# Kernel tuning notes

Hardware: AMD Instinct MI355X
Metric: run time of the kernel (lower is better)

## Reference

```python
import jax, jax.numpy as jnp
import numpy as np

B, T, U, E, INNER, VOCAB = 4, 400, 64, 320, 512, 1024

def setup_inputs() -> dict:
    key = jax.random.key(0)
    k1, k2, k3, k4, k5, k6 = jax.random.split(key, 6)
    enc_state = jax.random.normal(k1, (B, T, E), dtype=jnp.float32)
    dec_state = jax.random.normal(k2, (B, U, E), dtype=jnp.float32)
    # Linear(input_size=2E -> inner): torch stores W as (out, in)
    W1 = jax.random.normal(k3, (INNER, 2 * E), dtype=jnp.float32) * (1.0 / np.sqrt(2 * E))
    b1 = jax.random.normal(k4, (INNER,), dtype=jnp.float32) * 0.01
    W2 = jax.random.normal(k5, (VOCAB, INNER), dtype=jnp.float32) * (1.0 / np.sqrt(INNER))
    b2 = jax.random.normal(k6, (VOCAB,), dtype=jnp.float32) * 0.01
    return {"enc_state": enc_state, "dec_state": dec_state, "W1": W1, "b1": b1, "W2": W2, "b2": b2}

def reference(enc_state, dec_state, W1, b1, W2, b2):
    # Equivalent to: repeat enc to (B,T,U,E), dec to (B,T,U,E), concat -> Linear.
    # concat([enc,dec]) @ W1.T == enc @ W1[:, :E].T + dec @ W1[:, E:].T
    E_ = enc_state.shape[-1]
    enc_proj = jnp.einsum('bte,ie->bti', enc_state, W1[:, :E_])   # (B,T,inner)
    dec_proj = jnp.einsum('bue,ie->bui', dec_state, W1[:, E_:])   # (B,U,inner)
    h = jnp.tanh(enc_proj[:, :, None, :] + dec_proj[:, None, :, :] + b1)  # (B,T,U,inner)
    out = jnp.einsum('btui,vi->btuv', h, W2) + b2                  # (B,T,U,vocab)
    return out
```

## Files before the change

kernel.cpp:

```cpp
#include <hip/hip_runtime.h>

#define B_     4
#define T_     400
#define U_     64
#define E_     320
#define INNER_ 512
#define VOCAB_ 1024
#define M_     (B_ * T_ * U_)
#define BT_    (B_ * T_)
#define NROWS_ (BT_ + B_ * U_)

typedef __attribute__((ext_vector_type(8))) short short8;
typedef __attribute__((ext_vector_type(4))) float f32x4;

__device__ __forceinline__ unsigned short f2bf(float f) {
    union { float f; unsigned u; } v;
    v.f = f;
    unsigned u = v.u;
    u += 0x7fffu + ((u >> 16) & 1u);
    return (unsigned short)(u >> 16);
}

__device__ __forceinline__ float tanh_fast(float x) {
    float e = __expf(2.0f * x);
    return 1.0f - 2.0f / (e + 1.0f);
}

__device__ __forceinline__ void gload_lds16(const void* g, void* l) {
    __builtin_amdgcn_global_load_lds(
        (const __attribute__((address_space(1))) unsigned int*)g,
        (__attribute__((address_space(3))) unsigned int*)l,
        16, 0, 0);
}

#define PROJ_BLOCKS 232
#define CVT_BLOCKS  256

__global__ __launch_bounds__(256) void prep_kernel(
    const float* __restrict__ enc,
    const float* __restrict__ dec,
    const float* __restrict__ W1,
    const float* __restrict__ b1,
    const float* __restrict__ W2,
    float* __restrict__ proj,
    unsigned short* __restrict__ W2bf) {
    __shared__ float xs[8][E_];
    const int tid = threadIdx.x;

    if (blockIdx.x >= PROJ_BLOCKS) {
        const int i = ((blockIdx.x - PROJ_BLOCKS) * 256 + tid) * 8;
        float4 a = *(const float4*)(W2 + i);
        float4 b = *(const float4*)(W2 + i + 4);
        short8 o;
        o[0] = (short)f2bf(a.x); o[1] = (short)f2bf(a.y);
        o[2] = (short)f2bf(a.z); o[3] = (short)f2bf(a.w);
        o[4] = (short)f2bf(b.x); o[5] = (short)f2bf(b.y);
        o[6] = (short)f2bf(b.z); o[7] = (short)f2bf(b.w);
        *(short8*)(W2bf + i) = o;
        return;
    }

    const int r0 = blockIdx.x * 8;
    for (int i = tid; i < 8 * E_; i += 256) {
        const int rr = i / E_;
        const int cc = i - rr * E_;
        const int row = r0 + rr;
        const float* src = (row < BT_) ? (enc + row * E_)
                                       : (dec + (row - BT_) * E_);
        xs[rr][cc] = src[cc];
    }
    const int colbase = (r0 < BT_) ? 0 : E_;
    __syncthreads();

    for (int o = tid; o < INNER_; o += 256) {
        const float* w = W1 + o * (2 * E_) + colbase;
        float acc[8] = {};
        for (int c = 0; c < E_; c += 4) {
            float4 wv = *(const float4*)(w + c);
            #pragma unroll
            for (int rr = 0; rr < 8; ++rr) {
                float4 x = *(const float4*)(&xs[rr][c]);
                acc[rr] += wv.x * x.x + wv.y * x.y + wv.z * x.z + wv.w * x.w;
            }
        }
        const float badd = colbase ? b1[o] : 0.0f;
        #pragma unroll
        for (int rr = 0; rr < 8; ++rr)
            proj[(r0 + rr) * INNER_ + o] = acc[rr] + badd;
    }
}

__global__ __launch_bounds__(256) void hgen_kernel(
    const float* __restrict__ encp,
    const float* __restrict__ decp,
    unsigned short* __restrict__ hbf) {
    const int gid = blockIdx.x * 256 + threadIdx.x;
    const int r   = gid >> 6;
    const int kk  = (gid & 63) << 3;
    const int bt  = r >> 6;
    const int u   = r & 63;
    const int b   = bt / T_;
    const float* e = encp + bt * INNER_ + kk;
    const float* d = decp + (b * U_ + u) * INNER_ + kk;
    short8 o;
    #pragma unroll
    for (int i = 0; i < 2; ++i) {
        float4 e4 = *(const float4*)(e + i * 4);
        float4 d4 = *(const float4*)(d + i * 4);
        o[i * 4 + 0] = (short)f2bf(tanh_fast(e4.x + d4.x));
        o[i * 4 + 1] = (short)f2bf(tanh_fast(e4.y + d4.y));
        o[i * 4 + 2] = (short)f2bf(tanh_fast(e4.z + d4.z));
        o[i * 4 + 3] = (short)f2bf(tanh_fast(e4.w + d4.w));
    }
    *(short8*)(hbf + ((size_t)r << 9) + kk) = o;
}

#define JBM 128
#define JBN 128
#define JBK 32

__global__ __launch_bounds__(256) void joint_gemm_kernel(
    const unsigned short* __restrict__ hbf,
    const unsigned short* __restrict__ W2bf,
    const float* __restrict__ b2,
    float* __restrict__ out) {
    __shared__ unsigned short As[JBM * JBK];
    __shared__ unsigned short Bs[JBN * JBK];

    const int bid = blockIdx.x;
    const int c  = bid & 7;
    const int j  = bid >> 3;
    const int mt = (j & ~7) | c;
    const int nt = j & 7;
    const int m0 = mt * JBM;
    const int n0 = nt * JBN;

    const int tid  = threadIdx.x;
    const int wid  = tid >> 6;
    const int lane = tid & 63;
    const int wm   = (wid & 1) * 64;
    const int wn   = (wid >> 1) * 64;

    const int fr   = lane & 15;
    const int koff = (lane >> 4) * 8;

    f32x4 acc[4][4] = {};

    const char* hbase = (const char*)hbf;
    const char* wbase = (const char*)W2bf;

    for (int kt = 0; kt < INNER_; kt += JBK) {
        const int kb = kt * 2;
        #pragma unroll
        for (int c2 = 0; c2 < 2; ++c2) {
            const int p    = c2 * 4096 + tid * 16;
            const int r    = p >> 6;
            const int off  = p & 63;
            const int ldsb = c2 * 4096 + (wid << 10);
            gload_lds16(hbase + (((size_t)(m0 + r)) << 10) + kb + off,
                        (char*)As + ldsb);
            gload_lds16(wbase + (((size_t)(n0 + r)) << 10) + kb + off,
                        (char*)Bs + ldsb);
        }
        __syncthreads();

        short8 af[4], bfr[4];
        #pragma unroll
        for (int i = 0; i < 4; ++i)
            af[i] = *(const short8*)(As + (wm + fr + i * 16) * JBK + koff);
        #pragma unroll
        for (int i = 0; i < 4; ++i)
            bfr[i] = *(const short8*)(Bs + (wn + fr + i * 16) * JBK + koff);
        #pragma unroll
        for (int im = 0; im < 4; ++im)
            #pragma unroll
            for (int in = 0; in < 4; ++in)
                acc[im][in] = __builtin_amdgcn_mfma_f32_16x16x32_bf16(
                    af[im], bfr[in], acc[im][in], 0, 0, 0);

        __syncthreads();
    }

    const int rq = (lane >> 4) * 4;
    const int cl = lane & 15;
    #pragma unroll
    for (int in = 0; in < 4; ++in) {
        const int col = n0 + wn + in * 16 + cl;
        const float bias = b2[col];
        #pragma unroll
        for (int im = 0; im < 4; ++im) {
            const size_t rbase = (size_t)(m0 + wm + im * 16 + rq);
            #pragma unroll
            for (int r = 0; r < 4; ++r) {
                out[(rbase + r) * VOCAB_ + col] = acc[im][in][r] + bias;
            }
        }
    }
}

#define BM  128
#define BN  128
#define BK  32
#define LDA 40

__global__ __launch_bounds__(256) void joint_fb_kernel(
    const float* __restrict__ encp,
    const float* __restrict__ decp,
    const unsigned short* __restrict__ W2bf,
    const float* __restrict__ b2,
    float* __restrict__ out) {
    __shared__ unsigned short As[BM * LDA];
    __shared__ unsigned short Bs[BN * LDA];

    const int bid = blockIdx.x;
    const int c  = bid & 7;
    const int j  = bid >> 3;
    const int mt = (j & ~7) | c;
    const int nt = j & 7;
    const int m0 = mt * BM;
    const int n0 = nt * BN;

    const int tid  = threadIdx.x;
    const int wid  = tid >> 6;
    const int lane = tid & 63;
    const int wm   = (wid & 1) * 64;
    const int wn   = (wid >> 1) * 64;

    const int sr = tid >> 1;
    const int sk = (tid & 1) * 16;
    const int gr = m0 + sr;
    const int bt = gr >> 6;
    const int uu = gr & 63;
    const int bb = bt / T_;
    const float* eprow = encp + bt * INNER_;
    const float* dprow = decp + (bb * U_ + uu) * INNER_;
    const unsigned short* wrow = W2bf + (size_t)(n0 + sr) * INNER_;

    f32x4 acc[4][4] = {};

    for (int kt = 0; kt < INNER_; kt += BK) {
        const float* ep = eprow + kt + sk;
        const float* dp = dprow + kt + sk;
        short8 p0, p1;
        #pragma unroll
        for (int i = 0; i < 4; ++i) {
            float4 e4 = *(const float4*)(ep + i * 4);
            float4 d4 = *(const float4*)(dp + i * 4);
            unsigned short h0 = f2bf(tanh_fast(e4.x + d4.x));
            unsigned short h1 = f2bf(tanh_fast(e4.y + d4.y));
            unsigned short h2 = f2bf(tanh_fast(e4.z + d4.z));
            unsigned short h3 = f2bf(tanh_fast(e4.w + d4.w));
            if (i < 2) {
                p0[i * 4 + 0] = (short)h0; p0[i * 4 + 1] = (short)h1;
                p0[i * 4 + 2] = (short)h2; p0[i * 4 + 3] = (short)h3;
            } else {
                p1[(i - 2) * 4 + 0] = (short)h0; p1[(i - 2) * 4 + 1] = (short)h1;
                p1[(i - 2) * 4 + 2] = (short)h2; p1[(i - 2) * 4 + 3] = (short)h3;
            }
        }
        *(short8*)(As + sr * LDA + sk)     = p0;
        *(short8*)(As + sr * LDA + sk + 8) = p1;

        short8 w0 = *(const short8*)(wrow + kt + sk);
        short8 w1 = *(const short8*)(wrow + kt + sk + 8);
        *(short8*)(Bs + sr * LDA + sk)     = w0;
        *(short8*)(Bs + sr * LDA + sk + 8) = w1;

        __syncthreads();

        const int fr   = lane & 15;
        const int koff = (lane >> 4) * 8;
        short8 af[4], bfr[4];
        #pragma unroll
        for (int i = 0; i < 4; ++i)
            af[i] = *(const short8*)(As + (wm + fr + i * 16) * LDA + koff);
        #pragma unroll
        for (int i = 0; i < 4; ++i)
            bfr[i] = *(const short8*)(Bs + (wn + fr + i * 16) * LDA + koff);
        #pragma unroll
        for (int im = 0; im < 4; ++im)
            #pragma unroll
            for (int in = 0; in < 4; ++in)
                acc[im][in] = __builtin_amdgcn_mfma_f32_16x16x32_bf16(
                    af[im], bfr[in], acc[im][in], 0, 0, 0);

        __syncthreads();
    }

    const int rq = (lane >> 4) * 4;
    const int cl = lane & 15;
    #pragma unroll
    for (int in = 0; in < 4; ++in) {
        const int col = n0 + wn + in * 16 + cl;
        const float bias = b2[col];
        #pragma unroll
        for (int im = 0; im < 4; ++im) {
            const size_t rbase = (size_t)(m0 + wm + im * 16 + rq);
            #pragma unroll
            for (int r = 0; r < 4; ++r) {
                out[(rbase + r) * VOCAB_ + col] = acc[im][in][r] + bias;
            }
        }
    }
}

extern "C" void kernel_launch(void* const* d_in, const int* in_sizes, int n_in,
                              void* d_out, int out_size, void* d_ws, size_t ws_size,
                              hipStream_t stream) {
    const float* enc = (const float*)d_in[0];
    const float* dec = (const float*)d_in[1];
    const float* W1  = (const float*)d_in[2];
    const float* b1  = (const float*)d_in[3];
    const float* W2  = (const float*)d_in[4];
    const float* b2  = (const float*)d_in[5];
    float* out = (float*)d_out;

    const size_t PROJ_BYTES = (size_t)NROWS_ * INNER_ * sizeof(float);
    const size_t W2_BYTES   = (size_t)VOCAB_ * INNER_ * 2;
    const size_t H_BYTES    = (size_t)M_ * INNER_ * 2;

    float* proj = (float*)d_ws;
    float* encp = proj;
    float* decp = proj + (size_t)BT_ * INNER_;
    unsigned short* W2bf = (unsigned short*)((char*)d_ws + PROJ_BYTES);
    unsigned short* hbf  = (unsigned short*)((char*)d_ws + PROJ_BYTES + W2_BYTES);

    prep_kernel<<<PROJ_BLOCKS + CVT_BLOCKS, 256, 0, stream>>>(
        enc, dec, W1, b1, W2, proj, W2bf);

    const int grid = (M_ / JBM) * (VOCAB_ / JBN);

    if (ws_size >= PROJ_BYTES + W2_BYTES + H_BYTES) {
        hgen_kernel<<<(M_ * INNER_) / (8 * 256), 256, 0, stream>>>(encp, decp, hbf);
        joint_gemm_kernel<<<grid, 256, 0, stream>>>(hbf, W2bf, b2, out);
    } else {
        joint_fb_kernel<<<grid, 256, 0, stream>>>(encp, decp, W2bf, b2, out);
    }
}
```

Before: 658.8 us.

## Replace joint GEMM with 256x256 tiled pipelined kernel over pre-swizzled tile images

```diff
diff --git a/kernel.cpp b/kernel.cpp
--- a/kernel.cpp
+++ b/kernel.cpp
@@ -10,6 +10,10 @@
 #define BT_    (B_ * T_)
 #define NROWS_ (BT_ + B_ * U_)
 
+#define MT_    (M_ / 256)
+#define NT_    (VOCAB_ / 256)
+#define KT_    (INNER_ / 64)
+
 typedef __attribute__((ext_vector_type(8))) short short8;
 typedef __attribute__((ext_vector_type(4))) float f32x4;
 
@@ -31,6 +35,10 @@
         (const __attribute__((address_space(1))) unsigned int*)g,
         (__attribute__((address_space(3))) unsigned int*)l,
         16, 0, 0);
+}
+
+__device__ __forceinline__ int img_off(int r, int eb) {
+    return r * 128 + (eb ^ ((r & 7) << 4));
 }
 
 #define PROJ_BLOCKS 232
@@ -43,20 +51,23 @@
     const float* __restrict__ b1,
     const float* __restrict__ W2,
     float* __restrict__ proj,
-    unsigned short* __restrict__ W2bf) {
+    char* __restrict__ w2t) {
     __shared__ float xs[8][E_];
     const int tid = threadIdx.x;
 
     if (blockIdx.x >= PROJ_BLOCKS) {
-        const int i = ((blockIdx.x - PROJ_BLOCKS) * 256 + tid) * 8;
-        float4 a = *(const float4*)(W2 + i);
-        float4 b = *(const float4*)(W2 + i + 4);
+        const int gid = (blockIdx.x - PROJ_BLOCKS) * 256 + tid;
+        const int v  = gid >> 6;
+        const int kk = (gid & 63) * 8;
+        float4 a = *(const float4*)(W2 + v * INNER_ + kk);
+        float4 b = *(const float4*)(W2 + v * INNER_ + kk + 4);
         short8 o;
         o[0] = (short)f2bf(a.x); o[1] = (short)f2bf(a.y);
         o[2] = (short)f2bf(a.z); o[3] = (short)f2bf(a.w);
         o[4] = (short)f2bf(b.x); o[5] = (short)f2bf(b.y);
         o[6] = (short)f2bf(b.z); o[7] = (short)f2bf(b.w);
-        *(short8*)(W2bf + i) = o;
+        const int kt = kk >> 6, e0 = kk & 63, nt = v >> 8, vl = v & 255;
+        *(short8*)(w2t + (((size_t)(kt * NT_ + nt)) << 15) + img_off(vl, e0 * 2)) = o;
         return;
     }
 
@@ -93,7 +104,7 @@
 __global__ __launch_bounds__(256) void hgen_kernel(
     const float* __restrict__ encp,
     const float* __restrict__ decp,
-    unsigned short* __restrict__ hbf) {
+    char* __restrict__ hbf) {
     const int gid = blockIdx.x * 256 + threadIdx.x;
     const int r   = gid >> 6;
     const int kk  = (gid & 63) << 3;
@@ -112,194 +123,166 @@
         o[i * 4 + 2] = (short)f2bf(tanh_fast(e4.z + d4.z));
         o[i * 4 + 3] = (short)f2bf(tanh_fast(e4.w + d4.w));
     }
-    *(short8*)(hbf + ((size_t)r << 9) + kk) = o;
-}
-
-#define JBM 128
-#define JBN 128
-#define JBK 32
-
-__global__ __launch_bounds__(256) void joint_gemm_kernel(
-    const unsigned short* __restrict__ hbf,
-    const unsigned short* __restrict__ W2bf,
+    const int kt = kk >> 6, e0 = kk & 63, mt = r >> 8, rl = r & 255;
+    *(short8*)(hbf + (((size_t)(kt * MT_ + mt)) << 15) + img_off(rl, e0 * 2)) = o;
+}
+
+__global__ __launch_bounds__(512, 2) void joint8_kernel(
+    const char* __restrict__ himg,
+    const char* __restrict__ wimg,
     const float* __restrict__ b2,
     float* __restrict__ out) {
-    __shared__ unsigned short As[JBM * JBK];
-    __shared__ unsigned short Bs[JBN * JBK];
+    __shared__ __align__(16) char lds[131072];
 
     const int bid = blockIdx.x;
-    const int c  = bid & 7;
-    const int j  = bid >> 3;
-    const int mt = (j & ~7) | c;
-    const int nt = j & 7;
-    const int m0 = mt * JBM;
-    const int n0 = nt * JBN;
+    const int swz = (bid & 7) * (MT_ * NT_ / 8) + (bid >> 3);
+    const int mt = swz >> 2;
+    const int nt = swz & 3;
+    const int m0 = mt * 256;
+    const int n0 = nt * 256;
 
     const int tid  = threadIdx.x;
     const int wid  = tid >> 6;
     const int lane = tid & 63;
-    const int wm   = (wid & 1) * 64;
-    const int wn   = (wid >> 1) * 64;
-
+    const int wm   = (wid & 4) ? 128 : 0;
+    const int wn   = (wid & 3) * 64;
     const int fr   = lane & 15;
-    const int koff = (lane >> 4) * 8;
-
-    f32x4 acc[4][4] = {};
-
-    const char* hbase = (const char*)hbf;
-    const char* wbase = (const char*)W2bf;
-
-    for (int kt = 0; kt < INNER_; kt += JBK) {
-        const int kb = kt * 2;
-        #pragma unroll
-        for (int c2 = 0; c2 < 2; ++c2) {
-            const int p    = c2 * 4096 + tid * 16;
-            const int r    = p >> 6;
-            const int off  = p & 63;
-            const int ldsb = c2 * 4096 + (wid << 10);
-            gload_lds16(hbase + (((size_t)(m0 + r)) << 10) + kb + off,
-                        (char*)As + ldsb);
-            gload_lds16(wbase + (((size_t)(n0 + r)) << 10) + kb + off,
-                        (char*)Bs + ldsb);
+    const int q16  = lane >> 4;
+
+    f32x4 acc[8][4] = {};
+    short8 fa0[4][2], fa1[4][2], fb0[2][2], fb1[2][2];
+
+    auto stage = [&](int rho) {
+        const int t  = rho >> 2;
+        const int rr = rho & 3;
+        char* slot = lds + ((t & 1) << 16);
+        if (rr == 0 || rr == 3) {
+            const char* blk = himg + (((size_t)(t * MT_ + mt)) << 15);
+            const int ra = (rr == 3);
+            #pragma unroll
+            for (int j = 0; j < 2; ++j) {
+                const int off = ra * 8192 + j * 16384 + wid * 1024;
+                gload_lds16(blk + off + lane * 16, slot + off);
+            }
+        } else {
+            const char* blk = wimg + (((size_t)(t * NT_ + nt)) << 15);
+            const int rb = (rr == 2);
+            char* bslot = slot + 32768;
+            #pragma unroll
+            for (int j = 0; j < 2; ++j) {
+                const int off = j * 16384 + (wid >> 2) * 8192 + rb * 4096 + (wid & 3) * 1024;
+                gload_lds16(blk + off + lane * 16, bslot + off);
+            }
         }
-        __syncthreads();
-
-        short8 af[4], bfr[4];
-        #pragma unroll
-        for (int i = 0; i < 4; ++i)
-            af[i] = *(const short8*)(As + (wm + fr + i * 16) * JBK + koff);
-        #pragma unroll
-        for (int i = 0; i < 4; ++i)
-            bfr[i] = *(const short8*)(Bs + (wn + fr + i * 16) * JBK + koff);
-        #pragma unroll
-        for (int im = 0; im < 4; ++im)
-            #pragma unroll
-            for (int in = 0; in < 4; ++in)
-                acc[im][in] = __builtin_amdgcn_mfma_f32_16x16x32_bf16(
-                    af[im], bfr[in], acc[im][in], 0, 0, 0);
-
-        __syncthreads();
-    }
-
-    const int rq = (lane >> 4) * 4;
-    const int cl = lane & 15;
+    };
+
+    stage(0); stage(1); stage(2); stage(3); stage(4);
+
     #pragma unroll
-    for (int in = 0; in < 4; ++in) {
-        const int col = n0 + wn + in * 16 + cl;
+    for (int g = 0; g < 32; ++g) {
+        const int t = g >> 2;
+        const int c = g & 3;
+        if (g <= 27)      asm volatile("s_waitcnt vmcnt(6)" ::: "memory");
+        else if (g == 28) asm volatile("s_waitcnt vmcnt(4)" ::: "memory");
+        else if (g == 29) asm volatile("s_waitcnt vmcnt(2)" ::: "memory");
+        else              asm volatile("s_waitcnt vmcnt(0)" ::: "memory");
+        __builtin_amdgcn_s_barrier();
+        if (g + 5 < 32) stage(g + 5);
+
+        const char* Asl = lds + ((t & 1) << 16);
+        const char* Bsl = Asl + 32768;
+
+        if (c == 0) {
+            #pragma unroll
+            for (int i = 0; i < 4; ++i) {
+                const int R = wm + i * 16 + fr;
+                const int sw = (R & 7) << 4;
+                fa0[i][0] = *(const short8*)(Asl + R * 128 + ((q16 * 16) ^ sw));
+                fa0[i][1] = *(const short8*)(Asl + R * 128 + ((64 + q16 * 16) ^ sw));
+            }
+            #pragma unroll
+            for (int j = 0; j < 2; ++j) {
+                const int R = wn + j * 16 + fr;
+                const int sw = (R & 7) << 4;
+                fb0[j][0] = *(const short8*)(Bsl + R * 128 + ((q16 * 16) ^ sw));
+                fb0[j][1] = *(const short8*)(Bsl + R * 128 + ((64 + q16 * 16) ^ sw));
+            }
+            __builtin_amdgcn_s_setprio(1);
+            #pragma unroll
+            for (int i = 0; i < 4; ++i)
+                #pragma unroll
+                for (int j = 0; j < 2; ++j) {
+                    acc[i][j] = __builtin_amdgcn_mfma_f32_16x16x32_bf16(
+                        fa0[i][0], fb0[j][0], acc[i][j], 0, 0, 0);
+                    acc[i][j] = __builtin_amdgcn_mfma_f32_16x16x32_bf16(
+                        fa0[i][1], fb0[j][1], acc[i][j], 0, 0, 0);
+                }
+            __builtin_amdgcn_s_setprio(0);
+        } else if (c == 1) {
+            #pragma unroll
+            for (int j = 0; j < 2; ++j) {
+                const int R = wn + 32 + j * 16 + fr;
+                const int sw = (R & 7) << 4;
+                fb1[j][0] = *(const short8*)(Bsl + R * 128 + ((q16 * 16) ^ sw));
+                fb1[j][1] = *(const short8*)(Bsl + R * 128 + ((64 + q16 * 16) ^ sw));
+            }
+            __builtin_amdgcn_s_setprio(1);
+            #pragma unroll
+            for (int i = 0; i < 4; ++i)
+                #pragma unroll
+                for (int j = 0; j < 2; ++j) {
+                    acc[i][2 + j] = __builtin_amdgcn_mfma_f32_16x16x32_bf16(
+                        fa0[i][0], fb1[j][0], acc[i][2 + j], 0, 0, 0);
+                    acc[i][2 + j] = __builtin_amdgcn_mfma_f32_16x16x32_bf16(
+                        fa0[i][1], fb1[j][1], acc[i][2 + j], 0, 0, 0);
+                }
+            __builtin_amdgcn_s_setprio(0);
+        } else if (c == 2) {
+            #pragma unroll
+            for (int i = 0; i < 4; ++i) {
+                const int R = wm + 64 + i * 16 + fr;
+                const int sw = (R & 7) << 4;
+                fa1[i][0] = *(const short8*)(Asl + R * 128 + ((q16 * 16) ^ sw));
+                fa1[i][1] = *(const short8*)(Asl + R * 128 + ((64 + q16 * 16) ^ sw));
+            }
+            __builtin_amdgcn_s_setprio(1);
+            #pragma unroll
+            for (int i = 0; i < 4; ++i)
+                #pragma unroll
+                for (int j = 0; j < 2; ++j) {
+                    acc[4 + i][2 + j] = __builtin_amdgcn_mfma_f32_16x16x32_bf16(
+                        fa1[i][0], fb1[j][0], acc[4 + i][2 + j], 0, 0, 0);
+                    acc[4 + i][2 + j] = __builtin_amdgcn_mfma_f32_16x16x32_bf16(
+                        fa1[i][1], fb1[j][1], acc[4 + i][2 + j], 0, 0, 0);
+                }
+            __builtin_amdgcn_s_setprio(0);
+        } else {
+            __builtin_amdgcn_s_setprio(1);
+            #pragma unroll
+            for (int i = 0; i < 4; ++i)
+                #pragma unroll
+                for (int j = 0; j < 2; ++j) {
+                    acc[4 + i][j] = __builtin_amdgcn_mfma_f32_16x16x32_bf16(
+                        fa1[i][0], fb0[j][0], acc[4 + i][j], 0, 0, 0);
+                    acc[4 + i][j] = __builtin_amdgcn_mfma_f32_16x16x32_bf16(
+                        fa1[i][1], fb0[j][1], acc[4 + i][j], 0, 0, 0);
+                }
+            __builtin_amdgcn_s_setprio(0);
+        }
+    }
+
+    const int rq = q16 * 4;
+    const int cl = fr;
+    #pragma unroll
+    for (int cj = 0; cj < 4; ++cj) {
+        const int col = n0 + wn + (cj >> 1) * 32 + (cj & 1) * 16 + cl;
         const float bias = b2[col];
         #pragma unroll
-        for (int im = 0; im < 4; ++im) {
-            const size_t rbase = (size_t)(m0 + wm + im * 16 + rq);
-            #pragma unroll
-            for (int r = 0; r < 4; ++r) {
-                out[(rbase + r) * VOCAB_ + col] = acc[im][in][r] + bias;
-            }
-        }
-    }
-}
-
-#define BM  128
-#define BN  128
-#define BK  32
-#define LDA 40
-
-__global__ __launch_bounds__(256) void joint_fb_kernel(
-    const float* __restrict__ encp,
-    const float* __restrict__ decp,
-    const unsigned short* __restrict__ W2bf,
-    const float* __restrict__ b2,
-    float* __restrict__ out) {
-    __shared__ unsigned short As[BM * LDA];
-    __shared__ unsigned short Bs[BN * LDA];
-
-    const int bid = blockIdx.x;
-    const int c  = bid & 7;
-    const int j  = bid >> 3;
-    const int mt = (j & ~7) | c;
-    const int nt = j & 7;
-    const int m0 = mt * BM;
-    const int n0 = nt * BN;
-
-    const int tid  = threadIdx.x;
-    const int wid  = tid >> 6;
-    const int lane = tid & 63;
-    const int wm   = (wid & 1) * 64;
-    const int wn   = (wid >> 1) * 64;
-
-    const int sr = tid >> 1;
-    const int sk = (tid & 1) * 16;
-    const int gr = m0 + sr;
-    const int bt = gr >> 6;
-    const int uu = gr & 63;
-    const int bb = bt / T_;
-    const float* eprow = encp + bt * INNER_;
-    const float* dprow = decp + (bb * U_ + uu) * INNER_;
-    const unsigned short* wrow = W2bf + (size_t)(n0 + sr) * INNER_;
-
-    f32x4 acc[4][4] = {};
-
-    for (int kt = 0; kt < INNER_; kt += BK) {
-        const float* ep = eprow + kt + sk;
-        const float* dp = dprow + kt + sk;
-        short8 p0, p1;
-        #pragma unroll
-        for (int i = 0; i < 4; ++i) {
-            float4 e4 = *(const float4*)(ep + i * 4);
-            float4 d4 = *(const float4*)(dp + i * 4);
-            unsigned short h0 = f2bf(tanh_fast(e4.x + d4.x));
-            unsigned short h1 = f2bf(tanh_fast(e4.y + d4.y));
-            unsigned short h2 = f2bf(tanh_fast(e4.z + d4.z));
-            unsigned short h3 = f2bf(tanh_fast(e4.w + d4.w));
-            if (i < 2) {
-                p0[i * 4 + 0] = (short)h0; p0[i * 4 + 1] = (short)h1;
-                p0[i * 4 + 2] = (short)h2; p0[i * 4 + 3] = (short)h3;
-            } else {
-                p1[(i - 2) * 4 + 0] = (short)h0; p1[(i - 2) * 4 + 1] = (short)h1;
-                p1[(i - 2) * 4 + 2] = (short)h2; p1[(i - 2) * 4 + 3] = (short)h3;
-            }
-        }
-        *(short8*)(As + sr * LDA + sk)     = p0;
-        *(short8*)(As + sr * LDA + sk + 8) = p1;
-
-        short8 w0 = *(const short8*)(wrow + kt + sk);
-        short8 w1 = *(const short8*)(wrow + kt + sk + 8);
-        *(short8*)(Bs + sr * LDA + sk)     = w0;
-        *(short8*)(Bs + sr * LDA + sk + 8) = w1;
-
-        __syncthreads();
-
-        const int fr   = lane & 15;
-        const int koff = (lane >> 4) * 8;
-        short8 af[4], bfr[4];
-        #pragma unroll
-        for (int i = 0; i < 4; ++i)
-            af[i] = *(const short8*)(As + (wm + fr + i * 16) * LDA + koff);
-        #pragma unroll
-        for (int i = 0; i < 4; ++i)
-            bfr[i] = *(const short8*)(Bs + (wn + fr + i * 16) * LDA + koff);
-        #pragma unroll
-        for (int im = 0; im < 4; ++im)
-            #pragma unroll
-            for (int in = 0; in < 4; ++in)
-                acc[im][in] = __builtin_amdgcn_mfma_f32_16x16x32_bf16(
-                    af[im], bfr[in], acc[im][in], 0, 0, 0);
-
-        __syncthreads();
-    }
-
-    const int rq = (lane >> 4) * 4;
-    const int cl = lane & 15;
-    #pragma unroll
-    for (int in = 0; in < 4; ++in) {
-        const int col = n0 + wn + in * 16 + cl;
-        const float bias = b2[col];
-        #pragma unroll
-        for (int im = 0; im < 4; ++im) {
-            const size_t rbase = (size_t)(m0 + wm + im * 16 + rq);
-            #pragma unroll
-            for (int r = 0; r < 4; ++r) {
-                out[(rbase + r) * VOCAB_ + col] = acc[im][in][r] + bias;
-            }
+        for (int ri = 0; ri < 8; ++ri) {
+            const size_t rbase = (size_t)(m0 + wm + (ri >> 2) * 64 + (ri & 3) * 16 + rq);
+            #pragma unroll
+            for (int r = 0; r < 4; ++r)
+                out[(rbase + r) * VOCAB_ + col] = acc[ri][cj][r] + bias;
         }
     }
 }
@@ -317,23 +300,15 @@
 
     const size_t PROJ_BYTES = (size_t)NROWS_ * INNER_ * sizeof(float);
     const size_t W2_BYTES   = (size_t)VOCAB_ * INNER_ * 2;
-    const size_t H_BYTES    = (size_t)M_ * INNER_ * 2;
 
     float* proj = (float*)d_ws;
     float* encp = proj;
     float* decp = proj + (size_t)BT_ * INNER_;
-    unsigned short* W2bf = (unsigned short*)((char*)d_ws + PROJ_BYTES);
-    unsigned short* hbf  = (unsigned short*)((char*)d_ws + PROJ_BYTES + W2_BYTES);
+    char*  w2t  = (char*)d_ws + PROJ_BYTES;
+    char*  hbf  = w2t + W2_BYTES;
 
     prep_kernel<<<PROJ_BLOCKS + CVT_BLOCKS, 256, 0, stream>>>(
-        enc, dec, W1, b1, W2, proj, W2bf);
-
-    const int grid = (M_ / JBM) * (VOCAB_ / JBN);
-
-    if (ws_size >= PROJ_BYTES + W2_BYTES + H_BYTES) {
-        hgen_kernel<<<(M_ * INNER_) / (8 * 256), 256, 0, stream>>>(encp, decp, hbf);
-        joint_gemm_kernel<<<grid, 256, 0, stream>>>(hbf, W2bf, b2, out);
-    } else {
-        joint_fb_kernel<<<grid, 256, 0, stream>>>(encp, decp, W2bf, b2, out);
-    }
-}
+        enc, dec, W1, b1, W2, proj, w2t);
+    hgen_kernel<<<(M_ * INNER_) / (8 * 256), 256, 0, stream>>>(encp, decp, hbf);
+    joint8_kernel<<<MT_ * NT_, 512, 0, stream>>>(hbf, w2t, b2, out);
+}
```

Measured after the change: 615.1 us. 6.6% less time.
